# Kernel optimization log

Measured on AMD Instinct MI355X. Metric: run time of the kernel, lower is better.

## Reference

```python
import jax, jax.numpy as jnp
import numpy as np
from jax import lax

B, N, T, H, V, C = 256, 196, 26, 512, 12000, 1000


def setup_inputs() -> dict:
    key = jax.random.key(0)
    ks = jax.random.split(key, 24)
    g = lambda i, shape, s=0.02: jax.random.normal(ks[i], shape, jnp.float32) * s
    z = lambda *shape: jnp.zeros(shape, jnp.float32)
    return {
        "image": jax.random.normal(ks[0], (B, N, H), jnp.float32),
        "question": jax.random.randint(ks[1], (B, T), 0, V, jnp.int32),
        "embed_table": g(2, (V, H), 1.0),
        "W_img": g(3, (H, H)), "b_img": z(H),
        "W_uni": g(4, (1, H, H)), "b_uni": z(H),
        "W_bi": g(5, (2, H, H)), "b_bi": z(H),
        "W_tri": g(6, (3, H, H)), "b_tri": z(H),
        "lstm_k": g(7, (H, 4 * H)), "lstm_rk": g(8, (H, 4 * H)), "lstm_b": z(4 * H),
        "W_corr": g(9, (H, H)), "b_corr": z(H),
        "W_qe": g(10, (H, H)), "b_qe": z(H),
        "W_ie": g(11, (H, H)), "b_ie": z(H),
        "w_qa": g(12, (H, 1)), "b_qa": z(1),
        "w_ia": g(13, (H, 1)), "b_ia": z(1),
        "W_w": g(14, (H, H)), "b_w": z(H),
        "W_p": g(15, (2 * H, H)), "b_p": z(H),
        "W_s": g(16, (2 * H, H)), "b_s": z(H),
        "W_fc1": g(17, (H, 2 * H)), "b_fc1": z(2 * H),
        "W_fc": g(18, (2 * H, C)), "b_fc": z(C),
    }


def _conv1d(x, w, b, dil):
    # x: [B,T,H], w: [k, in, out] (WIO). TF 'same' padding == XLA SAME.
    y = lax.conv_general_dilated(x, w, window_strides=(1,), padding='SAME',
                                 rhs_dilation=(dil,),
                                 dimension_numbers=('NWC', 'WIO', 'NWC'))
    return y + b


def _lstm(x, k, rk, b):
    # Keras LSTM, gate order i,f,c,o; inference (dropout off).
    xp = jnp.einsum('bth,hg->btg', x, k) + b  # [B,T,4H]
    h0 = jnp.zeros((x.shape[0], rk.shape[0]), x.dtype)

    def step(carry, xt):
        h, c = carry
        zg = xt + h @ rk
        i, f, g, o = jnp.split(zg, 4, axis=-1)
        i, f, o = jax.nn.sigmoid(i), jax.nn.sigmoid(f), jax.nn.sigmoid(o)
        c = f * c + i * jnp.tanh(g)
        h = o * jnp.tanh(c)
        return (h, c), h

    _, hs = lax.scan(step, (h0, h0), jnp.swapaxes(xp, 0, 1))
    return jnp.swapaxes(hs, 0, 1)  # [B,T,H]


def _co_attention(img_feat, ques_feat, W_corr, b_corr, W_qe, b_qe, W_ie, b_ie,
                  w_qa, b_qa, w_ia, b_ia):
    img_corr = img_feat @ W_corr + b_corr                       # [B,N,H]
    wm = jnp.tanh(jnp.einsum('btd,bnd->btn', ques_feat, img_corr))  # affinity
    ques_embed = ques_feat @ W_qe + b_qe                        # [B,T,H]
    img_embed = img_feat @ W_ie + b_ie                          # [B,N,H]
    ques_sum = jnp.tanh(jnp.einsum('btn,bnd->btd', wm, img_embed) + ques_embed)
    ques_att = jax.nn.softmax((ques_sum @ w_qa + b_qa)[..., 0], axis=-1)  # [B,T]
    img_sum = jnp.tanh(jnp.einsum('btn,btd->bnd', wm, ques_embed) + img_embed)
    img_att = jax.nn.softmax((img_sum @ w_ia + b_ia)[..., 0], axis=-1)    # [B,N]
    q_feat = jnp.einsum('bt,btd->bd', ques_att, ques_feat)
    v_feat = jnp.einsum('bn,bnd->bd', img_att, img_feat)
    return v_feat, q_feat


def reference(image, question, embed_table, W_img, b_img, W_uni, b_uni, W_bi, b_bi,
              W_tri, b_tri, lstm_k, lstm_rk, lstm_b, W_corr, b_corr, W_qe, b_qe,
              W_ie, b_ie, w_qa, b_qa, w_ia, b_ia, W_w, b_w, W_p, b_p, W_s, b_s,
              W_fc1, b_fc1, W_fc, b_fc):
    img = jnp.tanh(image @ W_img + b_img)                       # [B,N,H]
    words = embed_table[question]                               # [B,T,H]
    uni = jnp.tanh(_conv1d(words, W_uni, b_uni, 1))
    bi = jnp.tanh(_conv1d(words, W_bi, b_bi, 2))
    tri = jnp.tanh(_conv1d(words, W_tri, b_tri, 2))
    phrase = jnp.tanh(jnp.maximum(jnp.maximum(uni, bi), tri))   # maxpool over 3 n-grams
    sentence = _lstm(phrase, lstm_k, lstm_rk, lstm_b)
    ca = lambda v, q: _co_attention(v, q, W_corr, b_corr, W_qe, b_qe, W_ie, b_ie,
                                    w_qa, b_qa, w_ia, b_ia)
    v_word, q_word = ca(img, words)
    v_phr, q_phr = ca(img, phrase)
    v_sent, q_sent = ca(img, sentence)
    h_w = jnp.tanh((q_word + v_word) @ W_w + b_w)
    h_p = jnp.tanh(jnp.concatenate([q_phr + v_phr, h_w], axis=1) @ W_p + b_p)
    h_s = jnp.tanh(jnp.concatenate([q_sent + v_sent, h_p], axis=1) @ W_s + b_s)
    fc1 = jax.nn.relu(h_s @ W_fc1 + b_fc1)
    return jax.nn.softmax(fc1 @ W_fc + b_fc, axis=-1)           # [B,C]
```

## Files before the change

### kernel.cpp

```cpp
#include <hip/hip_runtime.h>
#include <hip/hip_bf16.h>
#include <math.h>

#define Bq   256
#define Nimg 196
#define Tseq 26
#define Hd   512
#define H4   2048
#define Ccls 1000
#define KP   1536
#define MT3  19968

typedef int   int4v  __attribute__((ext_vector_type(4)));
typedef float f32x4  __attribute__((ext_vector_type(4)));

#define SWZ8(x) ((x) ^ (((x) >> 3) & 7))

__device__ __forceinline__ float fast_tanh(float x) {
    float e = __expf(2.0f * x);
    return 1.0f - 2.0f * __builtin_amdgcn_rcpf(e + 1.0f);
}
__device__ __forceinline__ float fast_sigmoid(float x) {
    return __builtin_amdgcn_rcpf(1.0f + __expf(-x));
}

__device__ __forceinline__ short f2bf(float x) {
    union { float f; unsigned u; } a; a.f = x;
    unsigned r = a.u + 0x7FFF + ((a.u >> 16) & 1);
    return (short)(r >> 16);
}
__device__ __forceinline__ float bf2f(short b) {
    union { float f; unsigned u; } a; a.u = ((unsigned)(unsigned short)b) << 16;
    return a.f;
}

__global__ void embed_kernel(const int* __restrict__ q, const float* __restrict__ table,
                             short* __restrict__ words2) {
    int row = blockIdx.x;
    int tok = q[row];
    int c4 = threadIdx.x * 4;
    float4 v = *reinterpret_cast<const float4*>(table + (size_t)tok * Hd + c4);
    short h0 = f2bf(v.x), h1 = f2bf(v.y), h2 = f2bf(v.z), h3 = f2bf(v.w);
    short l0 = f2bf(v.x - bf2f(h0)), l1 = f2bf(v.y - bf2f(h1));
    short l2 = f2bf(v.z - bf2f(h2)), l3 = f2bf(v.w - bf2f(h3));
    *reinterpret_cast<short4*>(words2 + (size_t)row * 1024 + c4) = make_short4(h0, h1, h2, h3);
    *reinterpret_cast<short4*>(words2 + (size_t)row * 1024 + 512 + c4) = make_short4(l0, l1, l2, l3);
}

__global__ void split_kernel(const float* __restrict__ X, short* __restrict__ X2) {
    int i4 = blockIdx.x * 256 + threadIdx.x;
    int m = i4 >> 7, c4 = (i4 & 127) * 4;
    float4 v = *reinterpret_cast<const float4*>(X + ((size_t)m << 9) + c4);
    short h0 = f2bf(v.x), h1 = f2bf(v.y), h2 = f2bf(v.z), h3 = f2bf(v.w);
    short l0 = f2bf(v.x - bf2f(h0)), l1 = f2bf(v.y - bf2f(h1));
    short l2 = f2bf(v.z - bf2f(h2)), l3 = f2bf(v.w - bf2f(h3));
    *reinterpret_cast<short4*>(X2 + (size_t)m * 1024 + c4) = make_short4(h0, h1, h2, h3);
    *reinterpret_cast<short4*>(X2 + (size_t)m * 1024 + 512 + c4) = make_short4(l0, l1, l2, l3);
}

__global__ __launch_bounds__(256) void wsplit_all_kernel(
    const float* __restrict__ W_img, const float* __restrict__ W_corr,
    const float* __restrict__ W_ie, const float* __restrict__ W_qe,
    const float* __restrict__ W_uni, const float* __restrict__ W_bi,
    const float* __restrict__ W_tri, const float* __restrict__ lstm_k,
    short* __restrict__ WimgT2, short* __restrict__ WcorrR2,
    short* __restrict__ WieT2, short* __restrict__ WqeT2,
    short* __restrict__ WconvT2, short* __restrict__ lkT2) {
    const int z = blockIdx.z;
    const int tid = threadIdx.x;
    const int k0 = blockIdx.y * 64;
    const size_t HK = (size_t)Hd * KP;
    if (z == 1) {
        const int n0 = blockIdx.x * 64;
        const int n = tid >> 2, ksub = (tid & 3) * 16;
        const float* src = W_corr + (size_t)(n0 + n) * Hd + k0 + ksub;
        size_t base = (size_t)(n0 + n) * KP + k0 + ksub;
        #pragma unroll
        for (int k = 0; k < 16; ++k) {
            float x = src[k];
            short h = f2bf(x);
            short l = f2bf(x - bf2f(h));
            WcorrR2[base + k] = h;
            WcorrR2[base + 512 + k] = h;
            WcorrR2[base + 1024 + k] = l;
        }
        return;
    }
    const float* W; short* WT2; int Nw, n0;
    if (z < 10) {
        Nw = Hd; n0 = blockIdx.x * 64;
        switch (z) {
            case 0: W = W_img;  WT2 = WimgT2;  break;
            case 2: W = W_ie;   WT2 = WieT2;   break;
            case 3: W = W_qe;   WT2 = WqeT2;   break;
            case 4: W = W_uni;                     WT2 = WconvT2 + 0 * HK; break;
            case 5: W = W_bi;                      WT2 = WconvT2 + 1 * HK; break;
            case 6: W = W_bi + (size_t)Hd * Hd;    WT2 = WconvT2 + 2 * HK; break;
            case 7: W = W_tri;                     WT2 = WconvT2 + 3 * HK; break;
            case 8: W = W_tri + (size_t)Hd * Hd;   WT2 = WconvT2 + 4 * HK; break;
            default:W = W_tri + 2 * (size_t)Hd * Hd; WT2 = WconvT2 + 5 * HK; break;
        }
    } else {
        Nw = H4; W = lstm_k; WT2 = lkT2;
        n0 = ((z - 10) * 8 + blockIdx.x) * 64;
    }
    __shared__ float tile[64][65];
    #pragma unroll
    for (int p = 0; p < 16; ++p) {
        int r = p * 4 + (tid >> 6);
        int c = tid & 63;
        tile[r][c] = W[(size_t)(k0 + r) * Nw + n0 + c];
    }
    __syncthreads();
    const int n = tid >> 2;
    const int ksub = (tid & 3) * 16;
    size_t base = (size_t)(n0 + n) * KP + k0 + ksub;
    #pragma unroll
    for (int k = 0; k < 16; ++k) {
        float x = tile[ksub + k][n];
        short h = f2bf(x);
        short l = f2bf(x - bf2f(h));
        WT2[base + k] = h;
        WT2[base + 512 + k] = h;
        WT2[base + 1024 + k] = l;
    }
}

__global__ __launch_bounds__(256) void qb_kernel(const short* __restrict__ Q2,
                                                 const float* __restrict__ b_corr,
                                                 float* __restrict__ qb) {
    const int tid = threadIdx.x, lane = tid & 63, wid = tid >> 6;
    const int r = blockIdx.x * 4 + wid;
    const short* row = Q2 + (size_t)r * 1024 + lane * 8;
    float v = 0.f;
    #pragma unroll
    for (int k = 0; k < 8; ++k) {
        float x = bf2f(row[k]) + bf2f(row[512 + k]);
        v += x * b_corr[lane * 8 + k];
    }
    #pragma unroll
    for (int off = 32; off; off >>= 1) v += __shfl_xor(v, off);
    if (lane == 0) qb[r] = v;
}

__device__ __forceinline__ void mfma16(f32x4& acc, int4v a, int4v b) {
    asm volatile("v_mfma_f32_16x16x32_bf16 %0, %1, %2, %0" : "+v"(acc) : "v"(a), "v"(b));
}

template <int ACT, int OUT, int SWZ>
__global__ __launch_bounds__(256) void mfma_gemm_kernel(
    const short* __restrict__ A2, const short* __restrict__ W2T,
    const float* __restrict__ bias, float* __restrict__ C, short* __restrict__ C2,
    int M, int N) {
    __shared__ __align__(16) short Asl[2][4096];
    __shared__ __align__(16) short Bsl[2][4096];
    const int tid = threadIdx.x;
    const int lane = tid & 63, wid = tid >> 6;
    int row0, col0;
    if (SWZ) {
        const int P8 = (M >> 7) >> 3;
        const int Cn = N >> 7;
        int L = blockIdx.x;
        int xcd = L & 7, slot = L >> 3;
        row0 = (xcd * P8 + slot / Cn) << 7;
        col0 = (slot % Cn) << 7;
    } else {
        row0 = blockIdx.y * 128;
        col0 = blockIdx.x * 128;
    }
    const int wm = wid >> 1, wn = wid & 1;
    const short* ab[2]; const short* bb[2]; int koff[2];
    #pragma unroll
    for (int c = 0; c < 2; ++c) {
        int d = c * 256 + tid;
        int s = SWZ8(d);
        int fr = s >> 6, r = (s >> 2) & 15, kb = s & 3;
        koff[c] = kb * 8;
        ab[c] = A2 + (size_t)(row0 + fr * 16 + r) * 1024;
        bb[c] = W2T + (size_t)(col0 + fr * 16 + r) * KP;
    }
    auto STAGE = [&](int buf, int k0) {
        #pragma unroll
        for (int c = 0; c < 2; ++c) {
            int kk = k0 + koff[c];
            int ka = kk >= 1024 ? kk - 1024 : kk;
            __builtin_amdgcn_global_load_lds(
                (const __attribute__((address_space(1))) void*)(ab[c] + ka),
                (__attribute__((address_space(3))) void*)(&Asl[buf][(c * 256 + wid * 64) * 8]),
                16, 0, 0);
            __builtin_amdgcn_global_load_lds(
                (const __attribute__((address_space(1))) void*)(bb[c] + kk),
                (__attribute__((address_space(3))) void*)(&Bsl[buf][(c * 256 + wid * 64) * 8]),
                16, 0, 0);
        }
    };
    f32x4 acc[4][4] = {};
    STAGE(0, 0);
    int cur = 0;
    for (int k0 = 0; k0 < KP; k0 += 32) {
        if (k0 + 32 < KP) {
            STAGE(cur ^ 1, k0 + 32);
            asm volatile("s_waitcnt vmcnt(4)" ::: "memory");
        } else {
            asm volatile("s_waitcnt vmcnt(0)" ::: "memory");
        }
        __builtin_amdgcn_s_barrier();
        __builtin_amdgcn_sched_barrier(0);
        int4v af[4], bfr[4];
        #pragma unroll
        for (int f = 0; f < 4; ++f) {
            int sa = (wm * 4 + f) * 64 + (lane & 15) * 4 + (lane >> 4);
            af[f] = *reinterpret_cast<const int4v*>(&Asl[cur][SWZ8(sa) * 8]);
            int sb = (wn * 4 + f) * 64 + (lane & 15) * 4 + (lane >> 4);
            bfr[f] = *reinterpret_cast<const int4v*>(&Bsl[cur][SWZ8(sb) * 8]);
        }
        #pragma unroll
        for (int i = 0; i < 4; ++i)
            #pragma unroll
            for (int j = 0; j < 4; ++j)
                mfma16(acc[i][j], af[i], bfr[j]);
        asm volatile("s_waitcnt lgkmcnt(0)" ::: "memory");
        __builtin_amdgcn_s_barrier();
        __builtin_amdgcn_sched_barrier(0);
        cur ^= 1;
    }
    asm volatile("s_nop 7\n\ts_nop 7" ::: "memory");
    #pragma unroll
    for (int i = 0; i < 4; ++i) {
        #pragma unroll
        for (int j = 0; j < 4; ++j) {
            int colj = col0 + wn * 64 + j * 16 + (lane & 15);
            float bv = bias ? bias[colj] : 0.f;
            #pragma unroll
            for (int r = 0; r < 4; ++r) {
                int row = row0 + wm * 64 + i * 16 + (lane >> 4) * 4 + r;
                float v = acc[i][j][r] + bv;
                if (ACT == 1) v = fast_tanh(v);
                if (OUT == 0) {
                    C[(size_t)row * N + colj] = v;
                } else {
                    short h = f2bf(v), l = f2bf(v - bf2f(h));
                    C2[(size_t)row * 1024 + colj] = h;
                    C2[(size_t)row * 1024 + 512 + colj] = l;
                }
            }
        }
    }
}

__global__ __launch_bounds__(256) void wm3_mfma_kernel(
    const short* __restrict__ Qc2, const short* __restrict__ img2,
    const float* __restrict__ qb, float* __restrict__ wm0, float* __restrict__ wm1,
    float* __restrict__ wm2) {
    __shared__ __align__(16) short Asl[2][4096];
    __shared__ __align__(16) short Bsl[2][4096];
    const int tid = threadIdx.x;
    const int lane = tid & 63, wid = tid >> 6;
    const int col0 = blockIdx.x * 128;
    const int b = blockIdx.y;
    const int wmq = wid >> 1, wn = wid & 1;
    const short* ab[2]; const short* bb[2]; int koff[2];
    #pragma unroll
    for (int c = 0; c < 2; ++c) {
        int d = c * 256 + tid;
        int s = SWZ8(d);
        int fr = s >> 6, r = (s >> 2) & 15, kb = s & 3;
        koff[c] = kb * 8;
        int arow = fr * 16 + r;
        int lvl = arow / 26, at = arow - lvl * 26;
        if (arow >= 78) { lvl = 0; at = 0; }
        ab[c] = Qc2 + ((size_t)lvl * (Bq * Tseq) + (size_t)(b * 26 + at)) * 1024;
        int brow = col0 + fr * 16 + r;
        if (brow > 195) brow = 195;
        bb[c] = img2 + ((size_t)(b * 196 + brow)) * 1024;
    }
    auto STAGE = [&](int buf, int k0) {
        #pragma unroll
        for (int c = 0; c < 2; ++c) {
            int kk = k0 + koff[c];
            int ka = kk >= 1024 ? kk - 1024 : kk;
            int kbv = kk >= 512 ? kk - 512 : kk;
            __builtin_amdgcn_global_load_lds(
                (const __attribute__((address_space(1))) void*)(ab[c] + ka),
                (__attribute__((address_space(3))) void*)(&Asl[buf][(c * 256 + wid * 64) * 8]),
                16, 0, 0);
            __builtin_amdgcn_global_load_lds(
                (const __attribute__((address_space(1))) void*)(bb[c] + kbv),
                (__attribute__((address_space(3))) void*)(&Bsl[buf][(c * 256 + wid * 64) * 8]),
                16, 0, 0);
        }
    };
    f32x4 acc[4][4] = {};
    STAGE(0, 0);
    int cur = 0;
    for (int k0 = 0; k0 < KP; k0 += 32) {
        if (k0 + 32 < KP) {
            STAGE(cur ^ 1, k0 + 32);
            asm volatile("s_waitcnt vmcnt(4)" ::: "memory");
        } else {
            asm volatile("s_waitcnt vmcnt(0)" ::: "memory");
        }
        __builtin_amdgcn_s_barrier();
        __builtin_amdgcn_sched_barrier(0);
        int4v af[4], bfr[4];
        #pragma unroll
        for (int f = 0; f < 4; ++f) {
            int sa = (wmq * 4 + f) * 64 + (lane & 15) * 4 + (lane >> 4);
            af[f] = *reinterpret_cast<const int4v*>(&Asl[cur][SWZ8(sa) * 8]);
            int sb = (wn * 4 + f) * 64 + (lane & 15) * 4 + (lane >> 4);
            bfr[f] = *reinterpret_cast<const int4v*>(&Bsl[cur][SWZ8(sb) * 8]);
        }
        #pragma unroll
        for (int i = 0; i < 4; ++i)
            #pragma unroll
            for (int j = 0; j < 4; ++j)
                mfma16(acc[i][j], af[i], bfr[j]);
        asm volatile("s_waitcnt lgkmcnt(0)" ::: "memory");
        __builtin_amdgcn_s_barrier();
        __builtin_amdgcn_sched_barrier(0);
        cur ^= 1;
    }
    asm volatile("s_nop 7\n\ts_nop 7" ::: "memory");
    #pragma unroll
    for (int i = 0; i < 4; ++i) {
        #pragma unroll
        for (int j = 0; j < 4; ++j) {
// ... 19 lines not shown
    int idx = blockIdx.x * 256 + threadIdx.x;
    int m = idx >> 9, c = idx & 511;
    int t = m % Tseq;
    const float* Ym = Y + (size_t)m * 3072;
    float u = Ym[c] + bu[c];
    float bv = bb[c];
    if (t > 0)  bv += Ym[-3072 + 512 + c];
    if (t < 25) bv += Ym[3072 + 1024 + c];
    float tv = Ym[2048 + c] + bt[c];
    if (t > 1)  tv += Ym[-6144 + 1536 + c];
    if (t < 24) tv += Ym[6144 + 2560 + c];
    float ph = fast_tanh(fmaxf(fmaxf(fast_tanh(u), fast_tanh(bv)), fast_tanh(tv)));
    short h = f2bf(ph), l = f2bf(ph - bf2f(h));
    phrase2[(size_t)m * 1024 + c] = h;
    phrase2[(size_t)m * 1024 + 512 + c] = l;
}

template <int ACT>
__global__ __launch_bounds__(256) void gemm_kernel(
    const float* __restrict__ A, int lda,
    const float* __restrict__ W, int ldw,
    const float* __restrict__ bias,
    float* __restrict__ C, int ldc,
    int M, int Ncols, int K) {
    __shared__ float As[16][68];
    __shared__ float Ws[16][68];
    const int tid = threadIdx.x;
    const int tx4 = (tid & 15) * 4, ty4 = (tid >> 4) * 4;
    const int row0 = blockIdx.y * 64, col0 = blockIdx.x * 64;
    const int am = tid >> 2, ak = (tid & 3) * 4;
    const int wk = tid >> 4, wc = (tid & 15) * 4;
    float acc[4][4] = {};
    for (int k0 = 0; k0 < K; k0 += 16) {
        {
            int gr = row0 + am;
            float4 v = make_float4(0.f, 0.f, 0.f, 0.f);
            if (gr < M) v = *reinterpret_cast<const float4*>(A + (size_t)gr * lda + k0 + ak);
            As[ak + 0][am] = v.x; As[ak + 1][am] = v.y; As[ak + 2][am] = v.z; As[ak + 3][am] = v.w;
        }
        {
            int gc = col0 + wc;
            const float* wp = W + (size_t)(k0 + wk) * ldw + gc;
            float4 v = make_float4(0.f, 0.f, 0.f, 0.f);
            if (gc + 3 < Ncols) v = *reinterpret_cast<const float4*>(wp);
            else {
                if (gc + 0 < Ncols) v.x = wp[0];
                if (gc + 1 < Ncols) v.y = wp[1];
                if (gc + 2 < Ncols) v.z = wp[2];
                if (gc + 3 < Ncols) v.w = wp[3];
            }
            Ws[wk][wc + 0] = v.x; Ws[wk][wc + 1] = v.y; Ws[wk][wc + 2] = v.z; Ws[wk][wc + 3] = v.w;
        }
        __syncthreads();
        #pragma unroll 4
        for (int kk = 0; kk < 16; ++kk) {
            float4 a4 = *reinterpret_cast<const float4*>(&As[kk][ty4]);
            float4 b4 = *reinterpret_cast<const float4*>(&Ws[kk][tx4]);
            float a[4] = {a4.x, a4.y, a4.z, a4.w};
            float b[4] = {b4.x, b4.y, b4.z, b4.w};
            #pragma unroll
            for (int i = 0; i < 4; ++i)
                #pragma unroll
                for (int j = 0; j < 4; ++j) acc[i][j] += a[i] * b[j];
        }
        __syncthreads();
    }
    #pragma unroll
    for (int i = 0; i < 4; ++i) {
        int r = row0 + ty4 + i;
        if (r >= M) continue;
        #pragma unroll
        for (int j = 0; j < 4; ++j) {
            int c = col0 + tx4 + j;
            if (c >= Ncols) continue;
            float v = acc[i][j];
            if (bias) v += bias[c];
            if (ACT == 1) v = fast_tanh(v);
            else if (ACT == 2) v = fmaxf(v, 0.f);
            C[(size_t)r * ldc + c] = v;
        }
    }
}

__global__ __launch_bounds__(256) void lstm_gemm_kernel(
    const float* __restrict__ h, const float* __restrict__ rk, float* __restrict__ zgp) {
    __shared__ float As[16][68];
    __shared__ float Ws[16][68];
    const int tid = threadIdx.x;
    const int tx4 = (tid & 15) * 4, ty4 = (tid >> 4) * 4;
    const int col0 = blockIdx.x * 64, row0 = blockIdx.y * 64, kb = blockIdx.z * 256;
    const int am = tid >> 2, ak = (tid & 3) * 4;
    const int wk = tid >> 4, wc = (tid & 15) * 4;
    float acc[4][4] = {};
    for (int k0 = kb; k0 < kb + 256; k0 += 16) {
        {
            float4 v = *reinterpret_cast<const float4*>(h + (size_t)(row0 + am) * Hd + k0 + ak);
            As[ak + 0][am] = v.x; As[ak + 1][am] = v.y; As[ak + 2][am] = v.z; As[ak + 3][am] = v.w;
        }
        {
            *reinterpret_cast<float4*>(&Ws[wk][wc]) =
                *reinterpret_cast<const float4*>(rk + (size_t)(k0 + wk) * H4 + col0 + wc);
        }
        __syncthreads();
        #pragma unroll 4
        for (int kk = 0; kk < 16; ++kk) {
            float4 a4 = *reinterpret_cast<const float4*>(&As[kk][ty4]);
            float4 b4 = *reinterpret_cast<const float4*>(&Ws[kk][tx4]);
            float a[4] = {a4.x, a4.y, a4.z, a4.w};
            float b[4] = {b4.x, b4.y, b4.z, b4.w};
            #pragma unroll
            for (int i = 0; i < 4; ++i)
                #pragma unroll
                for (int j = 0; j < 4; ++j) acc[i][j] += a[i] * b[j];
        }
        __syncthreads();
    }
    float* dst = zgp + (size_t)blockIdx.z * (Bq * H4);
    #pragma unroll
    for (int i = 0; i < 4; ++i) {
        int r = row0 + ty4 + i;
        *reinterpret_cast<float4*>(dst + (size_t)r * H4 + col0 + tx4) =
            make_float4(acc[i][0], acc[i][1], acc[i][2], acc[i][3]);
    }
}

__global__ __launch_bounds__(256) void lstm_gates_kernel(
    const float* __restrict__ zgp, const float* __restrict__ xp,
    float* __restrict__ c, float* __restrict__ h, short* __restrict__ sent2, int t) {
    int i = blockIdx.x * 256 + threadIdx.x;
    int b = i >> 9, hh = i & 511;
    const float* xr = xp + ((size_t)b * Tseq + t) * H4;
    float z[4];
    #pragma unroll
    for (int g = 0; g < 4; ++g) {
        float s = xr[g * 512 + hh];
        #pragma unroll
        for (int kc = 0; kc < 2; ++kc)
            s += zgp[(size_t)kc * (Bq * H4) + (size_t)b * H4 + g * 512 + hh];
        z[g] = s;
    }
    float ig = fast_sigmoid(z[0]);
    float fg = fast_sigmoid(z[1]);
    float gg = fast_tanh(z[2]);
    float og = fast_sigmoid(z[3]);
    float cv = fg * c[i] + ig * gg;
    c[i] = cv;
    float hv = og * fast_tanh(cv);
    h[i] = hv;
    short hb = f2bf(hv), lb = f2bf(hv - bf2f(hb));
    sent2[((size_t)b * Tseq + t) * 1024 + hh] = hb;
    sent2[((size_t)b * Tseq + t) * 1024 + 512 + hh] = lb;
}

__global__ __launch_bounds__(256) void qlog3_kernel(
    const float* __restrict__ wm0, const float* __restrict__ wm1, const float* __restrict__ wm2,
    const float* __restrict__ Ie, const float* __restrict__ qe0, const float* __restrict__ qe1,
    const float* __restrict__ qe2, const float* __restrict__ wqa, float* __restrict__ qlogp) {
    const int b = blockIdx.x, chunk = blockIdx.y;
    __shared__ float wms[3][Tseq][Nimg];
    __shared__ float red[4][40];
    const int tid = threadIdx.x;
    const float* wsrc[3] = {wm0, wm1, wm2};
    for (int e = tid; e < 3 * 1274; e += 256) {
        int c = e / 1274, r = e % 1274;
        *reinterpret_cast<float4*>(&wms[c][0][0] + 4 * r) =
            *reinterpret_cast<const float4*>(wsrc[c] + (size_t)b * (Tseq * Nimg) + 4 * r);
    }
    __syncthreads();
    const int hl = tid & 127, thalf = tid >> 7, tt0 = thalf * 13;
    const int h1 = chunk * 256 + hl, h2 = h1 + 128;
    float acc[3][13][2] = {};
    const float* iep1 = Ie + (size_t)b * Nimg * Hd + h1;
    const float* iep2 = Ie + (size_t)b * Nimg * Hd + h2;
    for (int n4 = 0; n4 < 49; ++n4) {
        float ieA0 = iep1[(size_t)(4 * n4 + 0) * Hd];
        float ieA1 = iep1[(size_t)(4 * n4 + 1) * Hd];
        float ieA2 = iep1[(size_t)(4 * n4 + 2) * Hd];
        float ieA3 = iep1[(size_t)(4 * n4 + 3) * Hd];
        float ieB0 = iep2[(size_t)(4 * n4 + 0) * Hd];
        float ieB1 = iep2[(size_t)(4 * n4 + 1) * Hd];
        float ieB2 = iep2[(size_t)(4 * n4 + 2) * Hd];
        float ieB3 = iep2[(size_t)(4 * n4 + 3) * Hd];
        #pragma unroll
        for (int c = 0; c < 3; ++c)
            #pragma unroll
            for (int tt = 0; tt < 13; ++tt) {
                float4 w4 = *reinterpret_cast<const float4*>(&wms[c][tt0 + tt][4 * n4]);
                acc[c][tt][0] += w4.x * ieA0 + w4.y * ieA1 + w4.z * ieA2 + w4.w * ieA3;
                acc[c][tt][1] += w4.x * ieB0 + w4.y * ieB1 + w4.z * ieB2 + w4.w * ieB3;
            }
    }
    const float wq1 = wqa[h1], wq2 = wqa[h2];
    const int lane = tid & 63, w = tid >> 6;
    const float* qes[3] = {qe0, qe1, qe2};
    #pragma unroll
    for (int c = 0; c < 3; ++c)
        #pragma unroll
        for (int tt = 0; tt < 13; ++tt) {
            int t = tt0 + tt;
            const float* qrow = qes[c] + ((size_t)(b * 26 + t)) * Hd;
            float v = fast_tanh(acc[c][tt][0] + qrow[h1]) * wq1 +
                      fast_tanh(acc[c][tt][1] + qrow[h2]) * wq2;
            #pragma unroll
            for (int off = 32; off; off >>= 1) v += __shfl_xor(v, off);
            if (lane == 0) red[w][c * 13 + tt] = v;
        }
    __syncthreads();
    if (tid < 39) {
        int c = tid / 13, tt = tid % 13;
        qlogp[((size_t)c * Bq + b) * (2 * 26) + chunk * 26 + tt] = red[0][tid] + red[1][tid];
    } else if (tid >= 64 && tid < 103) {
        int id = tid - 64;
        int c = id / 13, tt = id % 13;
        qlogp[((size_t)c * Bq + b) * (2 * 26) + chunk * 26 + 13 + tt] = red[2][id] + red[3][id];
    }
}

__global__ __launch_bounds__(256) void ilog3_kernel(
    const float* __restrict__ wmb, const float* __restrict__ qeb,
    const float* __restrict__ Ie, const float* __restrict__ wia,
    float* __restrict__ ilogp) {
    const int b = blockIdx.x, lvl = blockIdx.z;
    const int nbase = (blockIdx.y & 1) * 98, hc = blockIdx.y >> 1;
    const int hbase = hc * 256;
    const float* wm = wmb + (size_t)lvl * Bq * Tseq * Nimg;
    const float* qe = qeb + (size_t)lvl * Bq * Tseq * Hd;
    float* ilog = ilogp + (size_t)hc * (3 * Bq * Nimg) + (size_t)lvl * Bq * Nimg;
    __shared__ float qes[Tseq][260];
    __shared__ __align__(16) float wms[Tseq][104];
    const int tid = threadIdx.x;
    for (int e = tid; e < Tseq * 64; e += 256) {
        int t = e >> 6, q4 = (e & 63) * 4;
        *reinterpret_cast<float4*>(&qes[t][q4]) =
            *reinterpret_cast<const float4*>(qe + ((size_t)(b * 26 + t)) * Hd + hbase + q4);
// ... 149 lines not shown
                                                        float* __restrict__ out) {
    int b = blockIdx.x, tid = threadIdx.x;
    __shared__ float red[4];
    const float* lb = lg + (size_t)b * Ccls;
    float v[4]; float m = -INFINITY;
    #pragma unroll
    for (int k = 0; k < 4; ++k) {
        int j = tid + 256 * k;
        v[k] = (j < Ccls) ? lb[j] : -INFINITY;
        m = fmaxf(m, v[k]);
    }
    #pragma unroll
    for (int off = 32; off; off >>= 1) m = fmaxf(m, __shfl_xor(m, off));
    int lane = tid & 63, w = tid >> 6;
    if (lane == 0) red[w] = m;
    __syncthreads();
    m = fmaxf(fmaxf(red[0], red[1]), fmaxf(red[2], red[3]));
    __syncthreads();
    float e[4]; float s = 0.f;
    #pragma unroll
    for (int k = 0; k < 4; ++k) {
        int j = tid + 256 * k;
        e[k] = (j < Ccls) ? __expf(v[k] - m) : 0.f;
        s += e[k];
    }
    #pragma unroll
    for (int off = 32; off; off >>= 1) s += __shfl_xor(s, off);
    if (lane == 0) red[w] = s;
    __syncthreads();
    s = red[0] + red[1] + red[2] + red[3];
    float inv = 1.f / s;
    #pragma unroll
    for (int k = 0; k < 4; ++k) {
        int j = tid + 256 * k;
        if (j < Ccls) out[(size_t)b * Ccls + j] = e[k] * inv;
    }
}

extern "C" void kernel_launch(void* const* d_in, const int* in_sizes, int n_in,
                              void* d_out, int out_size, void* d_ws, size_t ws_size,
                              hipStream_t stream) {
    const float* image   = (const float*)d_in[0];
    const int*   question= (const int*)  d_in[1];
    const float* embed   = (const float*)d_in[2];
    const float* W_img   = (const float*)d_in[3];
    const float* b_img   = (const float*)d_in[4];
    const float* W_uni   = (const float*)d_in[5];
    const float* b_uni   = (const float*)d_in[6];
    const float* W_bi    = (const float*)d_in[7];
    const float* b_bi    = (const float*)d_in[8];
    const float* W_tri   = (const float*)d_in[9];
    const float* b_tri   = (const float*)d_in[10];
    const float* lstm_k  = (const float*)d_in[11];
    const float* lstm_rk = (const float*)d_in[12];
    const float* lstm_b  = (const float*)d_in[13];
    const float* W_corr  = (const float*)d_in[14];
    const float* b_corr  = (const float*)d_in[15];
    const float* W_qe    = (const float*)d_in[16];
    const float* b_qe    = (const float*)d_in[17];
    const float* W_ie    = (const float*)d_in[18];
    const float* b_ie    = (const float*)d_in[19];
    const float* w_qa    = (const float*)d_in[20];
    const float* w_ia    = (const float*)d_in[22];
    const float* W_w     = (const float*)d_in[24];
    const float* b_w     = (const float*)d_in[25];
    const float* W_p     = (const float*)d_in[26];
    const float* b_p     = (const float*)d_in[27];
    const float* W_s     = (const float*)d_in[28];
    const float* b_s     = (const float*)d_in[29];
    const float* W_fc1   = (const float*)d_in[30];
    const float* b_fc1   = (const float*)d_in[31];
    const float* W_fc    = (const float*)d_in[32];
    const float* b_fc    = (const float*)d_in[33];

    float* p = (float*)d_ws;
    size_t off = 0;
    auto take = [&](size_t n) { float* r = p + off; off += n; return r; };
    auto take_s = [&](size_t n) { short* r = (short*)(p + off); off += n / 2; return r; };
    float* bufB   = take((size_t)Bq * Nimg * Hd);
    float* xp     = take((size_t)Bq * Tseq * H4);
    float* wm0    = take((size_t)Bq * Tseq * Nimg);
    float* wm1    = take((size_t)Bq * Tseq * Nimg);
    float* wm2    = take((size_t)Bq * Tseq * Nimg);
    float* hbuf   = take((size_t)Bq * Hd);
    float* cbuf   = take((size_t)Bq * Hd);
    float* zgp    = take((size_t)2 * Bq * H4);
    float* qlogp  = take((size_t)3 * Bq * 4 * Tseq);
    float* qatt0  = take((size_t)Bq * Tseq);
    float* qatt1  = take((size_t)Bq * Tseq);
    float* qatt2  = take((size_t)Bq * Tseq);
    float* ilogp  = take((size_t)2 * 3 * Bq * Nimg);
    float* iatt0  = take((size_t)Bq * Nimg);
    float* iatt1  = take((size_t)Bq * Nimg);
    float* iatt2  = take((size_t)Bq * Nimg);
    float* qb     = take((size_t)MT3);
    short* imgS2   = take_s((size_t)Bq * Nimg * 1024);
    short* words2  = take_s((size_t)Bq * Tseq * 1024);
    short* phrase2 = take_s((size_t)Bq * Tseq * 1024);
    short* sentn2  = take_s((size_t)Bq * Tseq * 1024);
    short* WimgT2  = take_s((size_t)Hd * KP);
    short* WcorrR2 = take_s((size_t)Hd * KP);
    short* WieT2   = take_s((size_t)Hd * KP);
    short* WqeT2   = take_s((size_t)Hd * KP);
    short* WconvT2 = take_s((size_t)6 * Hd * KP);
    short* lkT2    = take_s((size_t)H4 * KP);

    float* qe0 = xp;
    float* qe1 = xp + (size_t)Bq * Tseq * Hd;
    float* qe2 = xp + 2 * (size_t)Bq * Tseq * Hd;
    float* s_part = xp + 3 * (size_t)Bq * Tseq * Hd;
    float* Y      = bufB;
    short* image2 = (short*)bufB;
    short* Qc2    = (short*)bufB;
    float* catb   = wm0;
    float* fc1b   = wm0 + (size_t)Bq * 2 * Hd;
    float* logits = wm0 + 2 * (size_t)Bq * 2 * Hd;
    float* s0     = wm1;
    float* s1     = wm1 + 1 * (size_t)Bq * Hd;
    float* s2     = wm1 + 2 * (size_t)Bq * Hd;
    float* hw     = wm1 + 3 * (size_t)Bq * Hd;
    float* hp     = wm1 + 4 * (size_t)Bq * Hd;
    float* hsv    = wm1 + 5 * (size_t)Bq * Hd;

    const int MI = Bq * Nimg;
    const int MT = Bq * Tseq;

    wsplit_all_kernel<<<dim3(8, 8, 14), 256, 0, stream>>>(
        W_img, W_corr, W_ie, W_qe, W_uni, W_bi, W_tri, lstm_k,
        WimgT2, WcorrR2, WieT2, WqeT2, WconvT2, lkT2);

    embed_kernel<<<MT, 128, 0, stream>>>(question, embed, words2);
    split_kernel<<<MI / 2, 256, 0, stream>>>(image, image2);
    mfma_gemm_kernel<1, 1, 1><<<dim3((MI / 128) * (Hd / 128)), 256, 0, stream>>>(
        image2, WimgT2, b_img, nullptr, imgS2, MI, Hd);
    mfma_gemm_kernel<0, 0, 0><<<dim3(3072 / 128, MT / 128), 256, 0, stream>>>(
        words2, WconvT2, nullptr, Y, nullptr, MT, 3072);
    conv_combine_kernel<<<(MT * Hd) / 256, 256, 0, stream>>>(Y, b_uni, b_bi, b_tri, phrase2);
    mfma_gemm_kernel<0, 0, 0><<<dim3(H4 / 128, MT / 128), 256, 0, stream>>>(
        phrase2, lkT2, lstm_b, xp, nullptr, MT, H4);
    hipMemsetAsync(hbuf, 0, (size_t)Bq * Hd * sizeof(float), stream);
    hipMemsetAsync(cbuf, 0, (size_t)Bq * Hd * sizeof(float), stream);
    for (int t = 0; t < Tseq; ++t) {
        lstm_gemm_kernel<<<dim3(32, 4, 2), 256, 0, stream>>>(hbuf, lstm_rk, zgp);
        lstm_gates_kernel<<<(Bq * Hd) / 256, 256, 0, stream>>>(zgp, xp, cbuf, hbuf, sentn2, t);
    }
    qb_kernel<<<MT3 / 4, 256, 0, stream>>>(words2, b_corr, qb);
    mfma_gemm_kernel<0, 1, 0><<<dim3(Hd / 128, MT3 / 128), 256, 0, stream>>>(
        words2, WcorrR2, nullptr, nullptr, Qc2, MT3, Hd);
    wm3_mfma_kernel<<<dim3(2, Bq), 256, 0, stream>>>(Qc2, imgS2, qb, wm0, wm1, wm2);
    mfma_gemm_kernel<0, 0, 1><<<dim3((MI / 128) * (Hd / 128)), 256, 0, stream>>>(
        imgS2, WieT2, b_ie, bufB, nullptr, MI, Hd);
    mfma_gemm_kernel<0, 0, 0><<<dim3(Hd / 128, MT3 / 128), 256, 0, stream>>>(
        words2, WqeT2, b_qe, qe0, nullptr, MT3, Hd);
    qlog3_kernel<<<dim3(Bq, 2), 256, 0, stream>>>(wm0, wm1, wm2, bufB, qe0, qe1, qe2, w_qa, qlogp);
    softmaxT_part_kernel<<<dim3(Bq, 3), 64, 0, stream>>>(qlogp, qatt0);
    ilog3_kernel<<<dim3(Bq, 4, 3), 256, 0, stream>>>(wm0, qe0, bufB, w_ia, ilogp);
    softmax_N_kernel<<<dim3(Bq, 3), 64, 0, stream>>>(ilogp, iatt0);
    feat3_kernel<<<dim3(Bq, 4), 256, 0, stream>>>(qatt0, qatt1, qatt2, iatt0, iatt1, iatt2,
                                                  words2, phrase2, sentn2, imgS2, s_part);
    feat_combine_kernel<<<(3 * Bq * Hd) / 256, 256, 0, stream>>>(s_part, s0, s1, s2);
    gemm_kernel<1><<<dim3(Hd / 64, Bq / 64), 256, 0, stream>>>(
        s0, Hd, W_w, Hd, b_w, hw, Hd, Bq, Hd, Hd);
    concat_kernel<<<(Bq * Hd) / 256, 256, 0, stream>>>(s1, hw, catb);
    gemm_kernel<1><<<dim3(Hd / 64, Bq / 64), 256, 0, stream>>>(
        catb, 2 * Hd, W_p, Hd, b_p, hp, Hd, Bq, Hd, 2 * Hd);
    concat_kernel<<<(Bq * Hd) / 256, 256, 0, stream>>>(s2, hp, catb);
    gemm_kernel<1><<<dim3(Hd / 64, Bq / 64), 256, 0, stream>>>(
        catb, 2 * Hd, W_s, Hd, b_s, hsv, Hd, Bq, Hd, 2 * Hd);
    gemm_kernel<2><<<dim3((2 * Hd) / 64, Bq / 64), 256, 0, stream>>>(
        hsv, Hd, W_fc1, 2 * Hd, b_fc1, fc1b, 2 * Hd, Bq, 2 * Hd, Hd);
    gemm_kernel<0><<<dim3((Ccls + 63) / 64, Bq / 64), 256, 0, stream>>>(
        fc1b, 2 * Hd, W_fc, Ccls, b_fc, logits, Ccls, Bq, Ccls, 2 * Hd);
    softmax_C_kernel<<<Bq, 256, 0, stream>>>(logits, (float*)d_out);
}
```

Measured before the change: 1.816 ms.

## Fuse LSTM recurrent GEMM with gate update via interleaved gate-column permutation

Permutes the recurrent and input weight columns so that each group of four adjacent output columns holds the i,f,g,o gates of one hidden unit. This lets the recurrent GEMM apply the gate nonlinearities and the cell/hidden update in its epilogue, replacing two launches per timestep with one. It also drops the split-K partial buffer and adds double-buffered h. The trade-off is that the full K=512 reduction now runs in each block over a grid of 128 blocks instead of 256, which lowers parallelism per step. Each call also pays for an extra permutation kernel and scratch buffer.

```diff
diff --git a/kernel.cpp b/kernel.cpp
--- a/kernel.cpp
+++ b/kernel.cpp
@@ -15,6 +15,7 @@
 typedef float f32x4  __attribute__((ext_vector_type(4)));
 
 #define SWZ8(x) ((x) ^ (((x) >> 3) & 7))
+#define PERM(c) ((((c) & 3) << 9) | ((c) >> 2))
 
 __device__ __forceinline__ float fast_tanh(float x) {
     float e = __expf(2.0f * x);
@@ -56,6 +57,12 @@
     short l2 = f2bf(v.z - bf2f(h2)), l3 = f2bf(v.w - bf2f(h3));
     *reinterpret_cast<short4*>(X2 + (size_t)m * 1024 + c4) = make_short4(h0, h1, h2, h3);
     *reinterpret_cast<short4*>(X2 + (size_t)m * 1024 + 512 + c4) = make_short4(l0, l1, l2, l3);
+}
+
+__global__ void rkperm_kernel(const float* __restrict__ rk, float* __restrict__ rkp) {
+    int i = blockIdx.x * 256 + threadIdx.x;
+    int k = i >> 11, c = i & 2047;
+    rkp[i] = rk[(size_t)k * H4 + PERM(c)];
 }
 
 __global__ __launch_bounds__(256) void wsplit_all_kernel(
@@ -87,6 +94,7 @@
         return;
     }
     const float* W; short* WT2; int Nw, n0;
+    bool perm = false;
     if (z < 10) {
         Nw = Hd; n0 = blockIdx.x * 64;
         switch (z) {
@@ -101,7 +109,7 @@
             default:W = W_tri + 2 * (size_t)Hd * Hd; WT2 = WconvT2 + 5 * HK; break;
         }
     } else {
-        Nw = H4; W = lstm_k; WT2 = lkT2;
+        Nw = H4; W = lstm_k; WT2 = lkT2; perm = true;
         n0 = ((z - 10) * 8 + blockIdx.x) * 64;
     }
     __shared__ float tile[64][65];
@@ -109,7 +117,8 @@
     for (int p = 0; p < 16; ++p) {
         int r = p * 4 + (tid >> 6);
         int c = tid & 63;
-        tile[r][c] = W[(size_t)(k0 + r) * Nw + n0 + c];
+        int col = perm ? PERM(n0 + c) : (n0 + c);
+        tile[r][c] = W[(size_t)(k0 + r) * Nw + col];
     }
     __syncthreads();
     const int n = tid >> 2;
@@ -427,24 +436,27 @@
     }
 }
 
-__global__ __launch_bounds__(256) void lstm_gemm_kernel(
-    const float* __restrict__ h, const float* __restrict__ rk, float* __restrict__ zgp) {
+__global__ __launch_bounds__(256) void lstm_step_kernel(
+    const float* __restrict__ hprev, const float* __restrict__ rkp,
+    const float* __restrict__ xp, const float* __restrict__ lb,
+    float* __restrict__ cbuf, float* __restrict__ hnext,
+    short* __restrict__ sent2, int t) {
     __shared__ float As[16][68];
     __shared__ float Ws[16][68];
     const int tid = threadIdx.x;
     const int tx4 = (tid & 15) * 4, ty4 = (tid >> 4) * 4;
-    const int col0 = blockIdx.x * 64, row0 = blockIdx.y * 64, kb = blockIdx.z * 256;
+    const int col0 = blockIdx.x * 64, row0 = blockIdx.y * 64;
     const int am = tid >> 2, ak = (tid & 3) * 4;
     const int wk = tid >> 4, wc = (tid & 15) * 4;
     float acc[4][4] = {};
-    for (int k0 = kb; k0 < kb + 256; k0 += 16) {
+    for (int k0 = 0; k0 < Hd; k0 += 16) {
         {
-            float4 v = *reinterpret_cast<const float4*>(h + (size_t)(row0 + am) * Hd + k0 + ak);
+            float4 v = *reinterpret_cast<const float4*>(hprev + (size_t)(row0 + am) * Hd + k0 + ak);
             As[ak + 0][am] = v.x; As[ak + 1][am] = v.y; As[ak + 2][am] = v.z; As[ak + 3][am] = v.w;
         }
         {
             *reinterpret_cast<float4*>(&Ws[wk][wc]) =
-                *reinterpret_cast<const float4*>(rk + (size_t)(k0 + wk) * H4 + col0 + wc);
+                *reinterpret_cast<const float4*>(rkp + (size_t)(k0 + wk) * H4 + col0 + wc);
         }
         __syncthreads();
         #pragma unroll 4
@@ -460,41 +472,26 @@
         }
         __syncthreads();
     }
-    float* dst = zgp + (size_t)blockIdx.z * (Bq * H4);
+    const int hh = (col0 + tx4) >> 2;
+    const float b0 = lb[hh], b1 = lb[512 + hh], b2 = lb[1024 + hh], b3 = lb[1536 + hh];
     #pragma unroll
     for (int i = 0; i < 4; ++i) {
         int r = row0 + ty4 + i;
-        *reinterpret_cast<float4*>(dst + (size_t)r * H4 + col0 + tx4) =
-            make_float4(acc[i][0], acc[i][1], acc[i][2], acc[i][3]);
-    }
-}
-
-__global__ __launch_bounds__(256) void lstm_gates_kernel(
-    const float* __restrict__ zgp, const float* __restrict__ xp,
-    float* __restrict__ c, float* __restrict__ h, short* __restrict__ sent2, int t) {
-    int i = blockIdx.x * 256 + threadIdx.x;
-    int b = i >> 9, hh = i & 511;
-    const float* xr = xp + ((size_t)b * Tseq + t) * H4;
-    float z[4];
-    #pragma unroll
-    for (int g = 0; g < 4; ++g) {
-        float s = xr[g * 512 + hh];
-        #pragma unroll
-        for (int kc = 0; kc < 2; ++kc)
-            s += zgp[(size_t)kc * (Bq * H4) + (size_t)b * H4 + g * 512 + hh];
-        z[g] = s;
-    }
-    float ig = fast_sigmoid(z[0]);
-    float fg = fast_sigmoid(z[1]);
-    float gg = fast_tanh(z[2]);
-    float og = fast_sigmoid(z[3]);
-    float cv = fg * c[i] + ig * gg;
-    c[i] = cv;
-    float hv = og * fast_tanh(cv);
-    h[i] = hv;
-    short hb = f2bf(hv), lb = f2bf(hv - bf2f(hb));
-    sent2[((size_t)b * Tseq + t) * 1024 + hh] = hb;
-    sent2[((size_t)b * Tseq + t) * 1024 + 512 + hh] = lb;
+        float4 xv = *reinterpret_cast<const float4*>(
+            xp + ((size_t)r * Tseq + t) * H4 + col0 + tx4);
+        float ig = fast_sigmoid(acc[i][0] + xv.x + b0);
+        float fg = fast_sigmoid(acc[i][1] + xv.y + b1);
+        float gg = fast_tanh(acc[i][2] + xv.z + b2);
+        float og = fast_sigmoid(acc[i][3] + xv.w + b3);
+        size_t ci = (size_t)r * Hd + hh;
+        float cv = fg * cbuf[ci] + ig * gg;
+        cbuf[ci] = cv;
+        float hv = og * fast_tanh(cv);
+        hnext[ci] = hv;
+        short hb = f2bf(hv), lbv = f2bf(hv - bf2f(hb));
+        sent2[((size_t)r * Tseq + t) * 1024 + hh] = hb;
+        sent2[((size_t)r * Tseq + t) * 1024 + 512 + hh] = lbv;
+    }
 }
 
 __global__ __launch_bounds__(256) void qlog3_kernel(
@@ -810,9 +807,10 @@
     float* wm0    = take((size_t)Bq * Tseq * Nimg);
     float* wm1    = take((size_t)Bq * Tseq * Nimg);
     float* wm2    = take((size_t)Bq * Tseq * Nimg);
-    float* hbuf   = take((size_t)Bq * Hd);
+    float* hbufA  = take((size_t)Bq * Hd);
+    float* hbufB  = take((size_t)Bq * Hd);
     float* cbuf   = take((size_t)Bq * Hd);
-    float* zgp    = take((size_t)2 * Bq * H4);
+    float* rkp    = take((size_t)Hd * H4);
     float* qlogp  = take((size_t)3 * Bq * 4 * Tseq);
     float* qatt0  = take((size_t)Bq * Tseq);
     float* qatt1  = take((size_t)Bq * Tseq);
@@ -856,6 +854,7 @@
     wsplit_all_kernel<<<dim3(8, 8, 14), 256, 0, stream>>>(
         W_img, W_corr, W_ie, W_qe, W_uni, W_bi, W_tri, lstm_k,
         WimgT2, WcorrR2, WieT2, WqeT2, WconvT2, lkT2);
+    rkperm_kernel<<<(Hd * H4) / 256, 256, 0, stream>>>(lstm_rk, rkp);
 
     embed_kernel<<<MT, 128, 0, stream>>>(question, embed, words2);
     split_kernel<<<MI / 2, 256, 0, stream>>>(image, image2);
@@ -865,12 +864,16 @@
         words2, WconvT2, nullptr, Y, nullptr, MT, 3072);
     conv_combine_kernel<<<(MT * Hd) / 256, 256, 0, stream>>>(Y, b_uni, b_bi, b_tri, phrase2);
     mfma_gemm_kernel<0, 0, 0><<<dim3(H4 / 128, MT / 128), 256, 0, stream>>>(
-        phrase2, lkT2, lstm_b, xp, nullptr, MT, H4);
-    hipMemsetAsync(hbuf, 0, (size_t)Bq * Hd * sizeof(float), stream);
+        phrase2, lkT2, nullptr, xp, nullptr, MT, H4);
+    hipMemsetAsync(hbufA, 0, (size_t)Bq * Hd * sizeof(float), stream);
     hipMemsetAsync(cbuf, 0, (size_t)Bq * Hd * sizeof(float), stream);
-    for (int t = 0; t < Tseq; ++t) {
-        lstm_gemm_kernel<<<dim3(32, 4, 2), 256, 0, stream>>>(hbuf, lstm_rk, zgp);
-        lstm_gates_kernel<<<(Bq * Hd) / 256, 256, 0, stream>>>(zgp, xp, cbuf, hbuf, sentn2, t);
+    {
+        float* hA = hbufA; float* hB = hbufB;
+        for (int t = 0; t < Tseq; ++t) {
+            lstm_step_kernel<<<dim3(32, 4), 256, 0, stream>>>(hA, rkp, xp, lstm_b,
+                                                              cbuf, hB, sentn2, t);
+            float* tmp = hA; hA = hB; hB = tmp;
+        }
     }
     qb_kernel<<<MT3 / 4, 256, 0, stream>>>(words2, b_corr, qb);
     mfma_gemm_kernel<0, 1, 0><<<dim3(Hd / 128, MT3 / 128), 256, 0, stream>>>(
```

Result: slower. 2.088 ms (+15.0%).

## Replace 128x128 MFMA GEMM with 256x256 eight-wave tile and K-64 staging

Applied to the files above, without the earlier changes.

The bf16-split MFMA GEMM moves from a 128x128 tile with four waves to a 256x256 tile with eight waves, a K step of 64, and double-buffered LDS slots. Staging of the next tile is spread across four sub-phases interleaved with compute, and the MFMA blocks are raised with s_setprio. The aim is more operand reuse per LDS byte and less global traffic per flop. In exchange it uses more LDS and registers per block (32 accumulators per wave), so occupancy drops, and the XCD-aware block swizzle is removed. Grids become small for some GEMMs: MT=6656 rows gives 26 row tiles, and N=512 gives only two column tiles.

```diff
diff --git a/kernel.cpp b/kernel.cpp
--- a/kernel.cpp
+++ b/kernel.cpp
@@ -147,101 +147,109 @@
     asm volatile("v_mfma_f32_16x16x32_bf16 %0, %1, %2, %0" : "+v"(acc) : "v"(a), "v"(b));
 }
 
-template <int ACT, int OUT, int SWZ>
-__global__ __launch_bounds__(256) void mfma_gemm_kernel(
+template <int ACT, int OUT>
+__global__ __launch_bounds__(512) void mfma_gemm8_kernel(
     const short* __restrict__ A2, const short* __restrict__ W2T,
     const float* __restrict__ bias, float* __restrict__ C, short* __restrict__ C2,
     int M, int N) {
-    __shared__ __align__(16) short Asl[2][4096];
-    __shared__ __align__(16) short Bsl[2][4096];
+    __shared__ __align__(16) short L[2][2][4][4096];
     const int tid = threadIdx.x;
     const int lane = tid & 63, wid = tid >> 6;
-    int row0, col0;
-    if (SWZ) {
-        const int P8 = (M >> 7) >> 3;
-        const int Cn = N >> 7;
-        int L = blockIdx.x;
-        int xcd = L & 7, slot = L >> 3;
-        row0 = (xcd * P8 + slot / Cn) << 7;
-        col0 = (slot % Cn) << 7;
-    } else {
-        row0 = blockIdx.y * 128;
-        col0 = blockIdx.x * 128;
-    }
-    const int wm = wid >> 1, wn = wid & 1;
-    const short* ab[2]; const short* bb[2]; int koff[2];
-    #pragma unroll
-    for (int c = 0; c < 2; ++c) {
-        int d = c * 256 + tid;
-        int s = SWZ8(d);
-        int fr = s >> 6, r = (s >> 2) & 15, kb = s & 3;
-        koff[c] = kb * 8;
-        ab[c] = A2 + (size_t)(row0 + fr * 16 + r) * 1024;
-        bb[c] = W2T + (size_t)(col0 + fr * 16 + r) * KP;
-    }
-    auto STAGE = [&](int buf, int k0) {
-        #pragma unroll
-        for (int c = 0; c < 2; ++c) {
-            int kk = k0 + koff[c];
-            int ka = kk >= 1024 ? kk - 1024 : kk;
-            __builtin_amdgcn_global_load_lds(
-                (const __attribute__((address_space(1))) void*)(ab[c] + ka),
-                (__attribute__((address_space(3))) void*)(&Asl[buf][(c * 256 + wid * 64) * 8]),
-                16, 0, 0);
-            __builtin_amdgcn_global_load_lds(
-                (const __attribute__((address_space(1))) void*)(bb[c] + kk),
-                (__attribute__((address_space(3))) void*)(&Bsl[buf][(c * 256 + wid * 64) * 8]),
-                16, 0, 0);
-        }
+    const int row0 = blockIdx.y * 256, col0 = blockIdx.x * 256;
+    const int wm = wid >> 2, wn = wid & 3;
+    const int sdec = SWZ8(tid);
+    const int frs = sdec >> 6, rs = (sdec >> 2) & 15, kb = sdec & 3;
+    const int koff = kb * 8;
+    const int aro = frs * 16 + rs;
+    const short* aptr[2]; const short* bptr[2];
+    aptr[0] = A2 + (size_t)(row0 + aro) * 1024;
+    aptr[1] = A2 + (size_t)(row0 + 128 + aro) * 1024;
+    bptr[0] = W2T + (size_t)(col0 + aro) * KP;
+    bptr[1] = W2T + (size_t)(col0 + 128 + aro) * KP;
+    const int ldso = wid * 64 * 8;
+    auto STAGE = [&](int slot, int tile, int p) {
+        int h = p & 1, kh = p >> 1;
+        int kk = tile * 64 + kh * 32 + koff;
+        int ka = kk >= 1024 ? kk - 1024 : kk;
+        __builtin_amdgcn_global_load_lds(
+            (const __attribute__((address_space(1))) void*)(aptr[h] + ka),
+            (__attribute__((address_space(3))) void*)(&L[slot][0][h * 2 + kh][ldso]),
+            16, 0, 0);
+        __builtin_amdgcn_global_load_lds(
+            (const __attribute__((address_space(1))) void*)(bptr[h] + kk),
+            (__attribute__((address_space(3))) void*)(&L[slot][1][h * 2 + kh][ldso]),
+            16, 0, 0);
     };
-    f32x4 acc[4][4] = {};
-    STAGE(0, 0);
-    int cur = 0;
-    for (int k0 = 0; k0 < KP; k0 += 32) {
-        if (k0 + 32 < KP) {
-            STAGE(cur ^ 1, k0 + 32);
-            asm volatile("s_waitcnt vmcnt(4)" ::: "memory");
-        } else {
-            asm volatile("s_waitcnt vmcnt(0)" ::: "memory");
-        }
-        __builtin_amdgcn_s_barrier();
-        __builtin_amdgcn_sched_barrier(0);
-        int4v af[4], bfr[4];
-        #pragma unroll
-        for (int f = 0; f < 4; ++f) {
-            int sa = (wm * 4 + f) * 64 + (lane & 15) * 4 + (lane >> 4);
-            af[f] = *reinterpret_cast<const int4v*>(&Asl[cur][SWZ8(sa) * 8]);
-            int sb = (wn * 4 + f) * 64 + (lane & 15) * 4 + (lane >> 4);
-            bfr[f] = *reinterpret_cast<const int4v*>(&Bsl[cur][SWZ8(sb) * 8]);
-        }
-        #pragma unroll
-        for (int i = 0; i < 4; ++i)
-            #pragma unroll
-            for (int j = 0; j < 4; ++j)
-                mfma16(acc[i][j], af[i], bfr[j]);
+    f32x4 acc[8][4] = {};
+    #pragma unroll
+    for (int p = 0; p < 4; ++p) STAGE(0, 0, p);
+    const int NT = KP / 64;
+    for (int t = 0; t < NT; ++t) {
+        const int sl = t & 1;
+        int4v bfr[4][2];
+        #pragma unroll
+        for (int p = 0; p < 4; ++p) {
+            if (p == 0) {
+                if (t + 1 < NT) {
+                    STAGE(sl ^ 1, t + 1, 0);
+                    asm volatile("s_waitcnt vmcnt(2)" ::: "memory");
+                } else {
+                    asm volatile("s_waitcnt vmcnt(0)" ::: "memory");
+                }
+                __builtin_amdgcn_s_barrier();
+                __builtin_amdgcn_sched_barrier(0);
+                #pragma unroll
+                for (int nf = 0; nf < 4; ++nf)
+                    #pragma unroll
+                    for (int kh = 0; kh < 2; ++kh) {
+                        int off = ((wn & 1) * 4 + nf) * 64 + (lane & 15) * 4 + (lane >> 4);
+                        bfr[nf][kh] = *reinterpret_cast<const int4v*>(
+                            &L[sl][1][(wn >> 1) * 2 + kh][SWZ8(off) * 8]);
+                    }
+            } else {
+                if (t + 1 < NT) STAGE(sl ^ 1, t + 1, p);
+            }
+            int4v af[2][2];
+            #pragma unroll
+            for (int i = 0; i < 2; ++i)
+                #pragma unroll
+                for (int kh = 0; kh < 2; ++kh) {
+                    int off = (p * 2 + i) * 64 + (lane & 15) * 4 + (lane >> 4);
+                    af[i][kh] = *reinterpret_cast<const int4v*>(
+                        &L[sl][0][wm * 2 + kh][SWZ8(off) * 8]);
+                }
+            __builtin_amdgcn_s_setprio(1);
+            #pragma unroll
+            for (int i = 0; i < 2; ++i)
+                #pragma unroll
+                for (int nf = 0; nf < 4; ++nf)
+                    #pragma unroll
+                    for (int kh = 0; kh < 2; ++kh)
+                        mfma16(acc[p * 2 + i][nf], af[i][kh], bfr[nf][kh]);
+            __builtin_amdgcn_s_setprio(0);
+        }
         asm volatile("s_waitcnt lgkmcnt(0)" ::: "memory");
         __builtin_amdgcn_s_barrier();
         __builtin_amdgcn_sched_barrier(0);
-        cur ^= 1;
     }
     asm volatile("s_nop 7\n\ts_nop 7" ::: "memory");
     #pragma unroll
-    for (int i = 0; i < 4; ++i) {
-        #pragma unroll
-        for (int j = 0; j < 4; ++j) {
-            int colj = col0 + wn * 64 + j * 16 + (lane & 15);
-            float bv = bias ? bias[colj] : 0.f;
+    for (int mf = 0; mf < 8; ++mf) {
+        #pragma unroll
+        for (int nf = 0; nf < 4; ++nf) {
+            int col = col0 + wn * 64 + nf * 16 + (lane & 15);
+            float bv = bias ? bias[col] : 0.f;
             #pragma unroll
             for (int r = 0; r < 4; ++r) {
-                int row = row0 + wm * 64 + i * 16 + (lane >> 4) * 4 + r;
-                float v = acc[i][j][r] + bv;
+                int row = row0 + wm * 128 + mf * 16 + (lane >> 4) * 4 + r;
+                float v = acc[mf][nf][r] + bv;
                 if (ACT == 1) v = fast_tanh(v);
                 if (OUT == 0) {
-                    C[(size_t)row * N + colj] = v;
+                    C[(size_t)row * N + col] = v;
                 } else {
                     short h = f2bf(v), l = f2bf(v - bf2f(h));
-                    C2[(size_t)row * 1024 + colj] = h;
-                    C2[(size_t)row * 1024 + 512 + colj] = l;
+                    C2[(size_t)row * 1024 + col] = h;
+                    C2[(size_t)row * 1024 + 512 + col] = l;
                 }
             }
         }
@@ -859,12 +867,12 @@
 
     embed_kernel<<<MT, 128, 0, stream>>>(question, embed, words2);
     split_kernel<<<MI / 2, 256, 0, stream>>>(image, image2);
-    mfma_gemm_kernel<1, 1, 1><<<dim3((MI / 128) * (Hd / 128)), 256, 0, stream>>>(
+    mfma_gemm8_kernel<1, 1><<<dim3(Hd / 256, MI / 256), 512, 0, stream>>>(
         image2, WimgT2, b_img, nullptr, imgS2, MI, Hd);
-    mfma_gemm_kernel<0, 0, 0><<<dim3(3072 / 128, MT / 128), 256, 0, stream>>>(
+    mfma_gemm8_kernel<0, 0><<<dim3(3072 / 256, MT / 256), 512, 0, stream>>>(
         words2, WconvT2, nullptr, Y, nullptr, MT, 3072);
     conv_combine_kernel<<<(MT * Hd) / 256, 256, 0, stream>>>(Y, b_uni, b_bi, b_tri, phrase2);
-    mfma_gemm_kernel<0, 0, 0><<<dim3(H4 / 128, MT / 128), 256, 0, stream>>>(
+    mfma_gemm8_kernel<0, 0><<<dim3(H4 / 256, MT / 256), 512, 0, stream>>>(
         phrase2, lkT2, lstm_b, xp, nullptr, MT, H4);
     hipMemsetAsync(hbuf, 0, (size_t)Bq * Hd * sizeof(float), stream);
     hipMemsetAsync(cbuf, 0, (size_t)Bq * Hd * sizeof(float), stream);
@@ -873,12 +881,12 @@
         lstm_gates_kernel<<<(Bq * Hd) / 256, 256, 0, stream>>>(zgp, xp, cbuf, hbuf, sentn2, t);
     }
     qb_kernel<<<MT3 / 4, 256, 0, stream>>>(words2, b_corr, qb);
-    mfma_gemm_kernel<0, 1, 0><<<dim3(Hd / 128, MT3 / 128), 256, 0, stream>>>(
+    mfma_gemm8_kernel<0, 1><<<dim3(Hd / 256, MT3 / 256), 512, 0, stream>>>(
         words2, WcorrR2, nullptr, nullptr, Qc2, MT3, Hd);
     wm3_mfma_kernel<<<dim3(2, Bq), 256, 0, stream>>>(Qc2, imgS2, qb, wm0, wm1, wm2);
-    mfma_gemm_kernel<0, 0, 1><<<dim3((MI / 128) * (Hd / 128)), 256, 0, stream>>>(
+    mfma_gemm8_kernel<0, 0><<<dim3(Hd / 256, MI / 256), 512, 0, stream>>>(
         imgS2, WieT2, b_ie, bufB, nullptr, MI, Hd);
-    mfma_gemm_kernel<0, 0, 0><<<dim3(Hd / 128, MT3 / 128), 256, 0, stream>>>(
+    mfma_gemm8_kernel<0, 0><<<dim3(Hd / 256, MT3 / 256), 512, 0, stream>>>(
         words2, WqeT2, b_qe, qe0, nullptr, MT3, Hd);
     qlog3_kernel<<<dim3(Bq, 2), 256, 0, stream>>>(wm0, wm1, wm2, bufB, qe0, qe1, qe2, w_qa, qlogp);
     softmaxT_part_kernel<<<dim3(Bq, 3), 64, 0, stream>>>(qlogp, qatt0);
```

Result: no change. 1.785 ms (-1.7%).
